# Kernel tuning notes

Measured on AMD Instinct MI355X. Metric: run time of the kernel, lower is better.

The kernel has to match this reference:

```python
import jax, jax.numpy as jnp
import numpy as np

DIM = 4096
HEADS = 32
HD = DIM // HEADS  # 128
SEQ = 2048
BSZ = 2
ALEN = 10
ROPE_THETA = 10000.0


def _make_freqs(seq, hd):
    inv = 1.0 / (ROPE_THETA ** (np.arange(0, hd, 2, dtype=np.float32) / hd))
    t = np.arange(seq, dtype=np.float32)
    ang = np.outer(t, inv)  # [seq, hd/2]
    return jnp.asarray(np.cos(ang)), jnp.asarray(np.sin(ang))


def setup_inputs() -> dict:
    key = jax.random.key(0)
    ks = jax.random.split(key, 8)
    s = 1.0 / np.sqrt(DIM)
    x = jax.random.normal(ks[0], (BSZ, SEQ, DIM), jnp.float32)
    wq = jax.random.normal(ks[1], (DIM, DIM), jnp.float32) * s  # [in, out]
    wk = jax.random.normal(ks[2], (DIM, DIM), jnp.float32) * s
    wv = jax.random.normal(ks[3], (DIM, DIM), jnp.float32) * s
    wo = jax.random.normal(ks[4], (DIM, DIM), jnp.float32) * s
    gate = 0.1 * jax.random.normal(ks[5], (1, HEADS, 1, 1), jnp.float32)
    adapter = jax.random.normal(ks[6], (1, ALEN, DIM), jnp.float32)
    freqs_cos, freqs_sin = _make_freqs(SEQ, HD)
    # causal additive mask, start_pos = 0
    mask = jnp.triu(jnp.full((1, 1, SEQ, SEQ), -1e9, jnp.float32), k=1)
    return {"x": x, "wq": wq, "wk": wk, "wv": wv, "wo": wo, "gate": gate,
            "adapter": adapter, "freqs_cos": freqs_cos, "freqs_sin": freqs_sin,
            "mask": mask, "start_pos": 0, "random_init": 0}


def _rope(t, cos, sin):
    # t: [b, s, H, hd]; cos/sin: [s, hd/2] -> broadcast (1, s, 1, hd/2)
    b, s, h, hd = t.shape
    t2 = t.reshape(b, s, h, hd // 2, 2)
    tr, ti = t2[..., 0], t2[..., 1]
    c = cos[None, :, None, :]
    sn = sin[None, :, None, :]
    orr = tr * c - ti * sn
    oi = tr * sn + ti * c
    return jnp.stack([orr, oi], axis=-1).reshape(b, s, h, hd)


def reference(x, wq, wk, wv, wo, gate, adapter, freqs_cos, freqs_sin, mask,
              start_pos, random_init):
    bsz, seqlen, dim = x.shape
    hd = 2 * freqs_cos.shape[-1]
    H = dim // hd
    L = adapter.shape[1]
    scale = 1.0 / jnp.sqrt(jnp.float32(hd))

    xq = (x @ wq).reshape(bsz, seqlen, H, hd)
    xk = (x @ wk).reshape(bsz, seqlen, H, hd)
    xv = (x @ wv).reshape(bsz, seqlen, H, hd)

    xq = _rope(xq, freqs_cos, freqs_sin)
    xk = _rope(xk, freqs_cos, freqs_sin)

    # adapter prefix K/V (no RoPE), shared across batch
    ak = (adapter @ wk).reshape(1, L, H, hd)  # [1, L, H, hd]
    av = (adapter @ wv).reshape(1, L, H, hd)

    # scores: normal keys masked causally; adapter keys unmasked (extra zeros)
    scores_n = jnp.einsum('bqhd,bkhd->bhqk', xq, xk) * scale + mask
    scores_a = jnp.einsum('bqhd,lhd->bhql', xq, ak[0]) * scale

    if random_init:
        # joint softmax over [adapter | normal] keys
        sc = jax.nn.softmax(jnp.concatenate([scores_a, scores_n], axis=-1), axis=-1)
        pa, pn = sc[..., :L], sc[..., L:]
    else:
        pa = jnp.tanh(gate) * jax.nn.softmax(scores_a, axis=-1)
        pn = jax.nn.softmax(scores_n, axis=-1)

    out = (jnp.einsum('bhql,lhd->bqhd', pa, av[0])
           + jnp.einsum('bhqk,bkhd->bqhd', pn, xv))
    out = out.reshape(bsz, seqlen, H * hd)
    return out @ wo
```

## Files before the change

kernel.cpp:

```cpp
#include <hip/hip_runtime.h>
#include <hip/hip_bf16.h>
#include <cstdint>

typedef float  f32x4  __attribute__((ext_vector_type(4)));
typedef __bf16 bf16x8 __attribute__((ext_vector_type(8)));
typedef __bf16 bf16x4 __attribute__((ext_vector_type(4)));
typedef __bf16 bf16x2 __attribute__((ext_vector_type(2)));

#define AS1 __attribute__((address_space(1)))
#define AS3 __attribute__((address_space(3)))

static constexpr int D   = 4096;
static constexpr int SEQ = 2048;
static constexpr int MX  = 4224;

__device__ __forceinline__ void gload_lds16(const void* g, void* l) {
  __builtin_amdgcn_global_load_lds((AS1 void*)(g), (AS3 void*)(l), 16, 0, 0);
}

__device__ __forceinline__ f32x4 mfma16(bf16x8 a, bf16x8 b, f32x4 c) {
  return __builtin_amdgcn_mfma_f32_16x16x32_bf16(a, b, c, 0, 0, 0);
}

__device__ __forceinline__ int xcd_chunk(int orig, int nwg) {
  int q = nwg >> 3, r = nwg & 7;
  int xcd = orig & 7, pos = orig >> 3;
  return (xcd < r ? xcd * (q + 1) : r * (q + 1) + (xcd - r) * q) + pos;
}

#define BARF() asm volatile("s_barrier" ::: "memory")

__global__ __launch_bounds__(256) void transpose_cast(const float* __restrict__ W,
                                                      __bf16* __restrict__ WT) {
  __shared__ float tile[64][65];
  const int t  = threadIdx.x;
  const int r0 = blockIdx.x * 64;
  const int c0 = blockIdx.y * 64;
#pragma unroll
  for (int p = 0; p < 4; ++p) {
    int e = p * 1024 + t * 4;
    int row = e >> 6, col = e & 63;
    f32x4 v = *(const f32x4*)(W + (size_t)(r0 + row) * D + c0 + col);
#pragma unroll
    for (int i = 0; i < 4; ++i) tile[row][col + i] = v[i];
  }
  __syncthreads();
#pragma unroll
  for (int p = 0; p < 2; ++p) {
    int e = p * 2048 + t * 8;
    int orow = e >> 6, ocol = e & 63;
    bf16x8 o;
#pragma unroll
    for (int i = 0; i < 8; ++i) o[i] = (__bf16)tile[ocol + i][orow];
    *(bf16x8*)(WT + (size_t)(c0 + orow) * D + r0 + ocol) = o;
  }
}

__global__ __launch_bounds__(256) void build_xa(const float* __restrict__ x,
                                                const float* __restrict__ ad,
                                                __bf16* __restrict__ xa) {
  int idx = blockIdx.x * 256 + threadIdx.x;
  int e = idx * 4;
  int row = e >> 12, col = e & 4095;
  f32x4 v = {};
  if (row < 4096)      v = *(const f32x4*)(x + (size_t)row * D + col);
  else if (row < 4106) v = *(const f32x4*)(ad + (size_t)(row - 4096) * D + col);
  bf16x4 o;
#pragma unroll
  for (int i = 0; i < 4; ++i) o[i] = (__bf16)v[i];
  *(bf16x4*)(xa + (size_t)row * D + col) = o;
}

template <int MODE>
__global__ __launch_bounds__(512, 2) void gemm256(const __bf16* __restrict__ A,
                                                  const __bf16* __restrict__ BT,
                                                  void* __restrict__ O0,
                                                  void* __restrict__ O1,
                                                  void* __restrict__ O2,
                                                  int Mt) {
  __shared__ __bf16 lds[65536];
  const int tid = threadIdx.x;
  const int wv = tid >> 6, ln = tid & 63;
  const int lg = ln >> 4, lr = ln & 15;

  const int nwg = gridDim.x;
  const int wgid = xcd_chunk(blockIdx.x, nwg);
  const int m0 = (wgid % Mt) * 256;
  const int n0 = (wgid / Mt) * 256;
  const int wm = (wv >> 2) * 128, wn = (wv & 3) * 64;

  auto stageHalf = [&](int k, int mat, int half) {
    const int slot = k & 1;
    const int kt = k * 64;
    const __bf16* base = mat ? BT + (size_t)(n0 + half * 128) * 4096
                             : A  + (size_t)(m0 + half * 128) * 4096;
#pragma unroll
    for (int i = 0; i < 2; ++i) {
      int c = i * 512 + tid;
      int r = c >> 3;
      int ch = (c & 7) ^ (r & 7);
      gload_lds16(base + (size_t)r * 4096 + kt + ch * 8,
                  lds + slot * 32768 + mat * 16384 + half * 8192 +
                      (i * 512 + wv * 64) * 8);
    }
  };

  f32x4 acc[8][4] = {};
  bf16x8 aLo[4][2], aHi[4][2], bLo[2][2], bHi[2][2];

  auto rdA = [&](const __bf16* pA, int mi, int kk) -> bf16x8 {
    int r = wm + mi * 16 + lr;
    int R = r & 127;
    int cw = (kk * 4 + lg) ^ (R & 7);
    return *(const bf16x8*)(pA + (r >> 7) * 8192 + R * 64 + cw * 8);
  };
  auto rdB = [&](const __bf16* pB, int ni, int kk) -> bf16x8 {
    int n = wn + ni * 16 + lr;
    int R = n & 127;
    int cw = (kk * 4 + lg) ^ (R & 7);
    return *(const bf16x8*)(pB + (n >> 7) * 8192 + R * 64 + cw * 8);
  };

  stageHalf(0, 0, 0);
  stageHalf(0, 1, 0);
  stageHalf(0, 0, 1);
  stageHalf(0, 1, 1);
  stageHalf(1, 0, 0);
  stageHalf(1, 1, 0);

  for (int k = 0; k < 63; ++k) {
    const int slot = k & 1;
    const __bf16* pA = lds + slot * 32768;
    const __bf16* pB = lds + slot * 32768 + 16384;

    stageHalf(k + 1, 0, 1);
    asm volatile("s_waitcnt vmcnt(8)" ::: "memory");
    BARF();
#pragma unroll
    for (int mi = 0; mi < 4; ++mi)
#pragma unroll
      for (int kk = 0; kk < 2; ++kk) aLo[mi][kk] = rdA(pA, mi, kk);
#pragma unroll
    for (int ni = 0; ni < 2; ++ni)
#pragma unroll
      for (int kk = 0; kk < 2; ++kk) bLo[ni][kk] = rdB(pB, ni, kk);
    __builtin_amdgcn_s_setprio(1);
#pragma unroll
    for (int kk = 0; kk < 2; ++kk)
#pragma unroll
      for (int mi = 0; mi < 4; ++mi)
#pragma unroll
        for (int ni = 0; ni < 2; ++ni)
          acc[mi][ni] = mfma16(aLo[mi][kk], bLo[ni][kk], acc[mi][ni]);
    __builtin_amdgcn_s_setprio(0);
    BARF();

    stageHalf(k + 1, 1, 1);
#pragma unroll
    for (int mi = 0; mi < 4; ++mi)
#pragma unroll
      for (int kk = 0; kk < 2; ++kk) aHi[mi][kk] = rdA(pA, mi + 4, kk);
    asm volatile("s_waitcnt vmcnt(8)" ::: "memory");
    BARF();
    __builtin_amdgcn_s_setprio(1);
#pragma unroll
    for (int kk = 0; kk < 2; ++kk)
#pragma unroll
      for (int mi = 0; mi < 4; ++mi)
#pragma unroll
        for (int ni = 0; ni < 2; ++ni)
          acc[mi + 4][ni] = mfma16(aHi[mi][kk], bLo[ni][kk], acc[mi + 4][ni]);
    __builtin_amdgcn_s_setprio(0);
    BARF();

    if (k + 2 < 64) stageHalf(k + 2, 0, 0);
#pragma unroll
    for (int ni = 0; ni < 2; ++ni)
#pragma unroll
      for (int kk = 0; kk < 2; ++kk) bHi[ni][kk] = rdB(pB, ni + 2, kk);
    BARF();
    __builtin_amdgcn_s_setprio(1);
#pragma unroll
    for (int kk = 0; kk < 2; ++kk)
#pragma unroll
      for (int mi = 0; mi < 4; ++mi)
#pragma unroll
        for (int ni = 0; ni < 2; ++ni)
          acc[mi + 4][ni + 2] = mfma16(aHi[mi][kk], bHi[ni][kk], acc[mi + 4][ni + 2]);
    __builtin_amdgcn_s_setprio(0);
    BARF();

    if (k + 2 < 64) stageHalf(k + 2, 1, 0);
    BARF();
    __builtin_amdgcn_s_setprio(1);
#pragma unroll
    for (int kk = 0; kk < 2; ++kk)
#pragma unroll
      for (int mi = 0; mi < 4; ++mi)
#pragma unroll
        for (int ni = 0; ni < 2; ++ni)
          acc[mi][ni + 2] = mfma16(aLo[mi][kk], bHi[ni][kk], acc[mi][ni + 2]);
    __builtin_amdgcn_s_setprio(0);
    BARF();
  }

  {
    const __bf16* pA = lds + (63 & 1) * 32768;
    const __bf16* pB = lds + (63 & 1) * 32768 + 16384;
    asm volatile("s_waitcnt vmcnt(0)" ::: "memory");
    BARF();
#pragma unroll
    for (int mi = 0; mi < 4; ++mi)
#pragma unroll
      for (int kk = 0; kk < 2; ++kk) aLo[mi][kk] = rdA(pA, mi, kk);
#pragma unroll
    for (int ni = 0; ni < 2; ++ni)
#pragma unroll
      for (int kk = 0; kk < 2; ++kk) bLo[ni][kk] = rdB(pB, ni, kk);
#pragma unroll
    for (int kk = 0; kk < 2; ++kk)
#pragma unroll
      for (int mi = 0; mi < 4; ++mi)
#pragma unroll
        for (int ni = 0; ni < 2; ++ni)
          acc[mi][ni] = mfma16(aLo[mi][kk], bLo[ni][kk], acc[mi][ni]);
#pragma unroll
    for (int mi = 0; mi < 4; ++mi)
#pragma unroll
      for (int kk = 0; kk < 2; ++kk) aHi[mi][kk] = rdA(pA, mi + 4, kk);
#pragma unroll
    for (int ni = 0; ni < 2; ++ni)
#pragma unroll
      for (int kk = 0; kk < 2; ++kk) bHi[ni][kk] = rdB(pB, ni + 2, kk);
#pragma unroll
    for (int kk = 0; kk < 2; ++kk)
#pragma unroll
      for (int mi = 0; mi < 4; ++mi)
#pragma unroll
        for (int ni = 0; ni < 2; ++ni) {
          acc[mi + 4][ni]     = mfma16(aHi[mi][kk], bLo[ni][kk], acc[mi + 4][ni]);
          acc[mi + 4][ni + 2] = mfma16(aHi[mi][kk], bHi[ni][kk], acc[mi + 4][ni + 2]);
          acc[mi][ni + 2]     = mfma16(aLo[mi][kk], bHi[ni][kk], acc[mi][ni + 2]);
        }
  }

  if constexpr (MODE == 0) {
    const int sel = n0 >> 12;
    __bf16* out = (sel == 0) ? (__bf16*)O0 : (sel == 1) ? (__bf16*)O1 : (__bf16*)O2;
    const int colb = n0 & 4095;
#pragma unroll
    for (int mi = 0; mi < 8; ++mi)
#pragma unroll
      for (int ni = 0; ni < 4; ++ni)
#pragma unroll
        for (int j = 0; j < 4; ++j) {
          int row = m0 + wm + mi * 16 + lg * 4 + j;
          int col = colb + wn + ni * 16 + lr;
          out[(size_t)row * 4096 + col] = (__bf16)acc[mi][ni][j];
        }
  } else {
    float* out = (float*)O0;
#pragma unroll
    for (int mi = 0; mi < 8; ++mi)
#pragma unroll
      for (int ni = 0; ni < 4; ++ni)
#pragma unroll
        for (int j = 0; j < 4; ++j) {
          int row = m0 + wm + mi * 16 + lg * 4 + j;
          int col = n0 + wn + ni * 16 + lr;
          out[(size_t)row * 4096 + col] = acc[mi][ni][j];
        }
  }
}

__global__ __launch_bounds__(256) void gemm_adapter(const __bf16* __restrict__ xa,
                                                    const __bf16* __restrict__ BT,
                                                    __bf16* __restrict__ kb,
                                                    __bf16* __restrict__ vb) {
  const int tid = threadIdx.x;
  const int wv = tid >> 6, ln = tid & 63;
  const int lg = ln >> 4, lr = ln & 15;
  const int col0 = blockIdx.x * 256 + wv * 64;
  f32x4 acc[4] = {};
  for (int kt = 0; kt < 4096; kt += 32) {
    bf16x8 a = *(const bf16x8*)(xa + (size_t)(4096 + lr) * 4096 + kt + lg * 8);
#pragma unroll
    for (int ni = 0; ni < 4; ++ni) {
      bf16x8 b = *(const bf16x8*)(BT + (size_t)(col0 + ni * 16 + lr) * 4096 +
                                  kt + lg * 8);
      acc[ni] = mfma16(a, b, acc[ni]);
    }
  }
#pragma unroll
  for (int ni = 0; ni < 4; ++ni)
#pragma unroll
    for (int j = 0; j < 4; ++j) {
      int row = 4096 + lg * 4 + j;
      int col = col0 + ni * 16 + lr;
      __bf16* out = (col < 4096) ? kb : vb;
      out[(size_t)row * 4096 + (col & 4095)] = (__bf16)acc[ni][j];
    }
}

__global__ __launch_bounds__(256) void rope_kernel(__bf16* __restrict__ q,
                                                   __bf16* __restrict__ k,
                                                   const float* __restrict__ fc,
                                                   const float* __restrict__ fs) {
  int row = blockIdx.x;
  __bf16* buf = blockIdx.y ? k : q;
  int t = threadIdx.x;
  int s = row & (SEQ - 1);
  int jb = (t & 7) * 8;
  const float* cp = fc + s * 64 + jb;
  const float* sp = fs + s * 64 + jb;
  __bf16* p = buf + (size_t)row * D + t * 16;
  bf16x8 v0 = *(const bf16x8*)p;
  bf16x8 v1 = *(const bf16x8*)(p + 8);
  bf16x8 o0, o1;
#pragma unroll
  for (int i = 0; i < 4; ++i) {
    float C = cp[i], Sn = sp[i];
    float re = (float)v0[2 * i], im = (float)v0[2 * i + 1];
    o0[2 * i]     = (__bf16)(re * C - im * Sn);
    o0[2 * i + 1] = (__bf16)(re * Sn + im * C);
  }
#pragma unroll
  for (int i = 0; i < 4; ++i) {
    float C = cp[4 + i], Sn = sp[4 + i];
    float re = (float)v1[2 * i], im = (float)v1[2 * i + 1];
    o1[2 * i]     = (__bf16)(re * C - im * Sn);
    o1[2 * i + 1] = (__bf16)(re * Sn + im * C);
  }
  *(bf16x8*)p = o0;
  *(bf16x8*)(p + 8) = o1;
}

__global__ __launch_bounds__(256) void transpose_v(const __bf16* __restrict__ V,
                                                   __bf16* __restrict__ VT) {
  __shared__ __bf16 tile[64][72];
  const int t  = threadIdx.x;
  const int r0 = blockIdx.x * 64;
  const int c0 = blockIdx.y * 64;
#pragma unroll
  for (int p = 0; p < 2; ++p) {
    int e = p * 2048 + t * 8;
    int row = e >> 6, col = e & 63;
    bf16x8 v8 = *(const bf16x8*)(V + (size_t)(r0 + row) * D + c0 + col);
#pragma unroll
    for (int i = 0; i < 8; ++i) tile[row][col + i] = v8[i];
  }
  __syncthreads();
#pragma unroll
  for (int p = 0; p < 2; ++p) {
    int e = p * 2048 + t * 8;
    int orow = e >> 6, ocol = e & 63;
    bf16x8 o;
#pragma unroll
    for (int i = 0; i < 8; ++i) o[i] = tile[ocol + i][orow];
    *(bf16x8*)(VT + (size_t)(c0 + orow) * MX + r0 + ocol) = o;
  }
}

__global__ __launch_bounds__(256) void attn_kernel(const __bf16* __restrict__ Q,
                                                   const __bf16* __restrict__ K,
                                                   const __bf16* __restrict__ VT,
                                                   const float* __restrict__ gate,
                                                   __bf16* __restrict__ Out) {
  __shared__ __bf16 Ks[2][64 * 128];
  __shared__ __bf16 Vs[2][128 * 64];
  __shared__ __bf16 Ps[4][32 * 64];

  const int tid = threadIdx.x;
  const int wv = tid >> 6, ln = tid & 63;
  const int lg = ln >> 4, lr = ln & 15;

  const int wgid = xcd_chunk(blockIdx.x, 512);
  const int px = wgid & 7;
  const int hb = wgid >> 3;
  const int h = hb & 31, b = hb >> 5;

  const float scale = 0.08838834764831845f;
  const float g = tanhf(gate[h]);

  auto stage = [&](int t, int buf) {
    const int kv0 = t * 64;
#pragma unroll
    for (int j = 0; j < 4; ++j) {
      int c = wv * 256 + j * 64 + ln;
      int rk = c >> 4, sck = (c & 15) ^ (rk & 7);
      gload_lds16(K + (size_t)(b * SEQ + kv0 + rk) * D + h * 128 + sck * 8,
                  Ks[buf] + (wv * 256 + j * 64) * 8);
      int rv = c >> 3, scv = (c & 7) ^ (rv & 7);
      gload_lds16(VT + (size_t)(h * 128 + rv) * MX + b * SEQ + kv0 + scv * 8,
                  Vs[buf] + (wv * 256 + j * 64) * 8);
    }
  };

  auto run_supertile = [&](int qt) {
    const int q0 = qt * 128;
    const int qbase = b * SEQ + q0 + wv * 32;

    bf16x8 qf[2][4];
#pragma unroll
    for (int mi = 0; mi < 2; ++mi)
#pragma unroll
      for (int kd = 0; kd < 4; ++kd)
        qf[mi][kd] = *(const bf16x8*)(Q + (size_t)(qbase + mi * 16 + lr) * D +
                                      h * 128 + kd * 32 + lg * 8);

    f32x4 O[2][8] = {};
    float mI2[2], lI2[2];
#pragma unroll
    for (int mi = 0; mi < 2; ++mi) { mI2[mi] = -1e30f; lI2[mi] = 0.f; }

    const int ntiles = 2 * qt + 2;
    stage(0, 0);

    for (int t = 0; t < ntiles; ++t) {
      const int cur = t & 1;
      const int kv0 = t * 64;
      if (t + 1 < ntiles) {
        stage(t + 1, cur ^ 1);
        asm volatile("s_waitcnt vmcnt(8)" ::: "memory");
      } else {
        asm volatile("s_waitcnt vmcnt(0)" ::: "memory");
      }
      __builtin_amdgcn_s_barrier();
      __builtin_amdgcn_sched_barrier(0);

      f32x4 S[2][4] = {};
      __builtin_amdgcn_s_setprio(1);
#pragma unroll
      for (int kd = 0; kd < 4; ++kd) {
        bf16x8 kf[4];
#pragma unroll
        for (int nf = 0; nf < 4; ++nf) {
          int kr = nf * 16 + lr;
          kf[nf] = *(const bf16x8*)(Ks[cur] + kr * 128 +
                                    (((kd * 4 + lg) ^ (kr & 7)) * 8));
        }
#pragma unroll
        for (int mi = 0; mi < 2; ++mi)
#pragma unroll
          for (int nf = 0; nf < 4; ++nf)
            S[mi][nf] = mfma16(kf[nf], qf[mi][kd], S[mi][nf]);
      }
      __builtin_amdgcn_s_setprio(0);

      float r2[2]; int grew = 0;
#pragma unroll
      for (int mi = 0; mi < 2; ++mi) {
        const int qg = q0 + wv * 32 + mi * 16 + lr;
        float mo = mI2[mi];
        float mt = -3e38f;
#pragma unroll
        for (int nf = 0; nf < 4; ++nf)
#pragma unroll
          for (int j = 0; j < 4; ++j) {
            int kvg = kv0 + nf * 16 + lg * 4 + j;
            float s = S[mi][nf][j] * scale;
            s = (kvg > qg) ? -1e30f : s;
            S[mi][nf][j] = s;
            mt = fmaxf(mt, s);
          }
        mt = fmaxf(mt, __shfl_xor(mt, 16));
        mt = fmaxf(mt, __shfl_xor(mt, 32));
        float mn = fmaxf(mo, mt);
        float ps = 0.f;
#pragma unroll
        for (int nf = 0; nf < 4; ++nf)
#pragma unroll
          for (int j = 0; j < 4; ++j) {
            float p = __expf(S[mi][nf][j] - mn);
            S[mi][nf][j] = p;
            ps += p;
          }
        ps += __shfl_xor(ps, 16);
        ps += __shfl_xor(ps, 32);
        float r = __expf(mo - mn);
        lI2[mi] = lI2[mi] * r + ps;
        mI2[mi] = mn;
        r2[mi] = r;
        grew |= (mn > mo) ? 1 : 0;
      }
      if (__any(grew)) {
#pragma unroll
        for (int mi = 0; mi < 2; ++mi)
#pragma unroll
          for (int j = 0; j < 4; ++j) {
            float rj = __shfl(r2[mi], lg * 4 + j);
#pragma unroll
            for (int n = 0; n < 8; ++n) O[mi][n][j] *= rj;
          }
      }

#pragma unroll
      for (int mi = 0; mi < 2; ++mi) {
        int q = mi * 16 + lr;
#pragma unroll
        for (int nf = 0; nf < 4; ++nf) {
          int kv = nf * 16 + lg * 4;
          bf16x4 pk;
#pragma unroll
          for (int j = 0; j < 4; ++j) pk[j] = (__bf16)S[mi][nf][j];
          *(bf16x4*)(Ps[wv] + q * 64 + (((kv >> 3) ^ (q & 7)) * 8) + (kv & 7)) = pk;
        }
      }

      __builtin_amdgcn_s_setprio(1);
#pragma unroll
      for (int kkv = 0; kkv < 2; ++kkv) {
        bf16x8 pf[2];
#pragma unroll
        for (int mi = 0; mi < 2; ++mi) {
          int prw = mi * 16 + lr;
          pf[mi] = *(const bf16x8*)(Ps[wv] + prw * 64 +
                                    (((kkv * 4 + lg) ^ (prw & 7)) * 8));
        }
#pragma unroll
        for (int n = 0; n < 8; ++n) {
          int vr = n * 16 + lr;
          bf16x8 vf = *(const bf16x8*)(Vs[cur] + vr * 64 +
                                       (((kkv * 4 + lg) ^ (vr & 7)) * 8));
#pragma unroll
          for (int mi = 0; mi < 2; ++mi) O[mi][n] = mfma16(pf[mi], vf, O[mi][n]);
        }
      }
      __builtin_amdgcn_s_setprio(0);

      __builtin_amdgcn_s_barrier();
      __builtin_amdgcn_sched_barrier(0);
    }

#pragma unroll
    for (int mi = 0; mi < 2; ++mi) {
      float inv = 1.0f / lI2[mi];
#pragma unroll
      for (int j = 0; j < 4; ++j) {
        float invj = __shfl(inv, lg * 4 + j);
#pragma unroll
        for (int n = 0; n < 8; ++n) O[mi][n][j] *= invj;
      }
    }

    {
      f32x4 Sa[2] = {};
#pragma unroll
      for (int kd = 0; kd < 4; ++kd) {
        bf16x8 kfa = *(const bf16x8*)(K + (size_t)(2 * SEQ + lr) * D +
                                      h * 128 + kd * 32 + lg * 8);
#pragma unroll
        for (int mi = 0; mi < 2; ++mi) Sa[mi] = mfma16(kfa, qf[mi][kd], Sa[mi]);
      }
#pragma unroll
      for (int mi = 0; mi < 2; ++mi) {
        float mt = -3e38f;
#pragma unroll
        for (int j = 0; j < 4; ++j) {
          int kv = lg * 4 + j;
          float s = Sa[mi][j] * scale;
          s = (kv >= 10) ? -1e30f : s;
          Sa[mi][j] = s;
          mt = fmaxf(mt, s);
        }
        mt = fmaxf(mt, __shfl_xor(mt, 16));
        mt = fmaxf(mt, __shfl_xor(mt, 32));
        float ps = 0.f;
#pragma unroll
        for (int j = 0; j < 4; ++j) {
          float p = __expf(Sa[mi][j] - mt);
          Sa[mi][j] = p;
          ps += p;
        }
        ps += __shfl_xor(ps, 16);
        ps += __shfl_xor(ps, 32);
        float gs = g / ps;
        int q = mi * 16 + lr;
        int kv = lg * 4;
        bf16x4 pk, z = {};
#pragma unroll
        for (int j = 0; j < 4; ++j) pk[j] = (__bf16)(Sa[mi][j] * gs);
        *(bf16x4*)(Ps[wv] + q * 64 + (((kv >> 3) ^ (q & 7)) * 8) + (kv & 7)) = pk;
        int kv2 = 16 + kv;
        *(bf16x4*)(Ps[wv] + q * 64 + (((kv2 >> 3) ^ (q & 7)) * 8) + (kv2 & 7)) = z;
      }
      bf16x8 pfa[2];
#pragma unroll
      for (int mi = 0; mi < 2; ++mi) {
        int prw = mi * 16 + lr;
        pfa[mi] = *(const bf16x8*)(Ps[wv] + prw * 64 + ((lg ^ (prw & 7)) * 8));
      }
#pragma unroll
      for (int n = 0; n < 8; ++n) {
        bf16x8 vfa = *(const bf16x8*)(VT + (size_t)(h * 128 + n * 16 + lr) * MX +
                                      2 * SEQ + lg * 8);
#pragma unroll
        for (int mi = 0; mi < 2; ++mi) O[mi][n] = mfma16(pfa[mi], vfa, O[mi][n]);
      }
    }

#pragma unroll
    for (int mi = 0; mi < 2; ++mi)
#pragma unroll
      for (int n = 0; n < 8; ++n)
#pragma unroll
        for (int j = 0; j < 4; ++j)
          Out[(size_t)(qbase + mi * 16 + lg * 4 + j) * D + h * 128 + n * 16 + lr] =
              (__bf16)O[mi][n][j];
  };

  run_supertile(15 - px);
  run_supertile(px);
}

extern "C" void kernel_launch(void* const* d_in, const int* in_sizes, int n_in,
                              void* d_out, int out_size, void* d_ws, size_t ws_size,
                              hipStream_t stream) {
  const float* x    = (const float*)d_in[0];
  const float* wq   = (const float*)d_in[1];
  const float* wk   = (const float*)d_in[2];
  const float* wv   = (const float*)d_in[3];
  const float* wo   = (const float*)d_in[4];
  const float* gate = (const float*)d_in[5];
  const float* ad   = (const float*)d_in[6];
  const float* fc   = (const float*)d_in[7];
  const float* fs   = (const float*)d_in[8];

  const size_t WSZ = (size_t)D * D * 2;
  const size_t XSZ = (size_t)MX * D * 2;
  if (ws_size < 4 * WSZ + XSZ + WSZ + 3 * XSZ) return;

  char* w = (char*)d_ws;
  size_t off = 0;
  auto alloc = [&](size_t sz) { void* p = w + off; off += sz; return p; };
  __bf16* wqT = (__bf16*)alloc(WSZ);
  __bf16* wkT = (__bf16*)alloc(WSZ);
  __bf16* wvT = (__bf16*)alloc(WSZ);
  __bf16* woT = (__bf16*)alloc(WSZ);
  __bf16* xa  = (__bf16*)alloc(XSZ);
  __bf16* qb  = (__bf16*)alloc(WSZ);
  __bf16* kb  = (__bf16*)alloc(XSZ);
  __bf16* vb  = (__bf16*)alloc(XSZ);
  __bf16* vT  = (__bf16*)alloc(XSZ);
  __bf16* attn = vb;

  dim3 blk(256);
  transpose_cast<<<dim3(64, 64), blk, 0, stream>>>(wq, wqT);
  transpose_cast<<<dim3(64, 64), blk, 0, stream>>>(wk, wkT);
  transpose_cast<<<dim3(64, 64), blk, 0, stream>>>(wv, wvT);
  transpose_cast<<<dim3(64, 64), blk, 0, stream>>>(wo, woT);
  build_xa<<<dim3(16896), blk, 0, stream>>>(x, ad, xa);

  gemm256<0><<<dim3(16 * 48), dim3(512), 0, stream>>>(xa, wqT, qb, kb, vb, 16);
  gemm_adapter<<<dim3(32), blk, 0, stream>>>(xa, wkT, kb, vb);

  rope_kernel<<<dim3(4096, 2), blk, 0, stream>>>(qb, kb, fc, fs);
  transpose_v<<<dim3(66, 64), blk, 0, stream>>>(vb, vT);

  attn_kernel<<<dim3(512), blk, 0, stream>>>(qb, kb, vT, gate, attn);

  gemm256<1><<<dim3(16 * 16), dim3(512), 0, stream>>>(attn, woT, d_out, nullptr, nullptr, 16);
}
```

Before: 850.8 us.

## Fuse RoPE and V transpose into QKV GEMM epilogue, batch weight transposes

Applies RoPE to Q and K inside the QKV GEMM epilogue, using a lane shuffle to pair real and imaginary parts. V is written straight into transposed layout, so the separate rope and transpose_v kernels and their round trips through global memory are removed. The four weight transpose-cast launches become one launch with a z dimension. In exchange the epilogue does more work, reads the frequency tables, and the transposed V stores are narrow strided writes that may coalesce poorly.

```diff
diff --git a/kernel.cpp b/kernel.cpp
--- a/kernel.cpp
+++ b/kernel.cpp
@@ -30,9 +30,15 @@
 
 #define BARF() asm volatile("s_barrier" ::: "memory")
 
-__global__ __launch_bounds__(256) void transpose_cast(const float* __restrict__ W,
-                                                      __bf16* __restrict__ WT) {
+__global__ __launch_bounds__(256) void transpose_cast4(const float* __restrict__ w0,
+                                                       const float* __restrict__ w1,
+                                                       const float* __restrict__ w2,
+                                                       const float* __restrict__ w3,
+                                                       __bf16* __restrict__ WT) {
   __shared__ float tile[64][65];
+  const float* W = (blockIdx.z == 0) ? w0 : (blockIdx.z == 1) ? w1
+                 : (blockIdx.z == 2) ? w2 : w3;
+  __bf16* dst = WT + (size_t)blockIdx.z * D * D;
   const int t  = threadIdx.x;
   const int r0 = blockIdx.x * 64;
   const int c0 = blockIdx.y * 64;
@@ -52,7 +58,7 @@
     bf16x8 o;
 #pragma unroll
     for (int i = 0; i < 8; ++i) o[i] = (__bf16)tile[ocol + i][orow];
-    *(bf16x8*)(WT + (size_t)(c0 + orow) * D + r0 + ocol) = o;
+    *(bf16x8*)(dst + (size_t)(c0 + orow) * D + r0 + ocol) = o;
   }
 }
 
@@ -77,6 +83,8 @@
                                                   void* __restrict__ O0,
                                                   void* __restrict__ O1,
                                                   void* __restrict__ O2,
+                                                  const float* __restrict__ FC,
+                                                  const float* __restrict__ FS,
                                                   int Mt) {
   __shared__ __bf16 lds[65536];
   const int tid = threadIdx.x;
@@ -246,18 +254,42 @@
 
   if constexpr (MODE == 0) {
     const int sel = n0 >> 12;
-    __bf16* out = (sel == 0) ? (__bf16*)O0 : (sel == 1) ? (__bf16*)O1 : (__bf16*)O2;
     const int colb = n0 & 4095;
-#pragma unroll
-    for (int mi = 0; mi < 8; ++mi)
-#pragma unroll
-      for (int ni = 0; ni < 4; ++ni)
+    if (sel < 2) {
+      __bf16* out = sel ? (__bf16*)O1 : (__bf16*)O0;
+#pragma unroll
+      for (int mi = 0; mi < 8; ++mi)
 #pragma unroll
         for (int j = 0; j < 4; ++j) {
           int row = m0 + wm + mi * 16 + lg * 4 + j;
+          int s = row & (SEQ - 1);
+#pragma unroll
+          for (int ni = 0; ni < 4; ++ni) {
+            int col = colb + wn + ni * 16 + lr;
+            int fi = (col & 127) >> 1;
+            float c  = FC[s * 64 + fi];
+            float sn = FS[s * 64 + fi];
+            float v = acc[mi][ni][j];
+            float p = __shfl_xor(v, 1);
+            float o = (lr & 1) ? (p * sn + v * c) : (v * c - p * sn);
+            out[(size_t)row * 4096 + col] = (__bf16)o;
+          }
+        }
+    } else {
+      __bf16* vT = (__bf16*)O2;
+#pragma unroll
+      for (int mi = 0; mi < 8; ++mi) {
+        int row0 = m0 + wm + mi * 16 + lg * 4;
+#pragma unroll
+        for (int ni = 0; ni < 4; ++ni) {
           int col = colb + wn + ni * 16 + lr;
-          out[(size_t)row * 4096 + col] = (__bf16)acc[mi][ni][j];
-        }
+          bf16x4 pk;
+#pragma unroll
+          for (int j = 0; j < 4; ++j) pk[j] = (__bf16)acc[mi][ni][j];
+          *(bf16x4*)(vT + (size_t)col * MX + row0) = pk;
+        }
+      }
+    }
   } else {
     float* out = (float*)O0;
 #pragma unroll
@@ -276,7 +308,7 @@
 __global__ __launch_bounds__(256) void gemm_adapter(const __bf16* __restrict__ xa,
                                                     const __bf16* __restrict__ BT,
                                                     __bf16* __restrict__ kb,
-                                                    __bf16* __restrict__ vb) {
+                                                    __bf16* __restrict__ vT) {
   const int tid = threadIdx.x;
   const int wv = tid >> 6, ln = tid & 63;
   const int lg = ln >> 4, lr = ln & 15;
@@ -297,68 +329,9 @@
     for (int j = 0; j < 4; ++j) {
       int row = 4096 + lg * 4 + j;
       int col = col0 + ni * 16 + lr;
-      __bf16* out = (col < 4096) ? kb : vb;
-      out[(size_t)row * 4096 + (col & 4095)] = (__bf16)acc[ni][j];
-    }
-}
-
-__global__ __launch_bounds__(256) void rope_kernel(__bf16* __restrict__ q,
-                                                   __bf16* __restrict__ k,
-                                                   const float* __restrict__ fc,
-                                                   const float* __restrict__ fs) {
-  int row = blockIdx.x;
-  __bf16* buf = blockIdx.y ? k : q;
-  int t = threadIdx.x;
-  int s = row & (SEQ - 1);
-  int jb = (t & 7) * 8;
-  const float* cp = fc + s * 64 + jb;
-  const float* sp = fs + s * 64 + jb;
-  __bf16* p = buf + (size_t)row * D + t * 16;
-  bf16x8 v0 = *(const bf16x8*)p;
-  bf16x8 v1 = *(const bf16x8*)(p + 8);
-  bf16x8 o0, o1;
-#pragma unroll
-  for (int i = 0; i < 4; ++i) {
-    float C = cp[i], Sn = sp[i];
-    float re = (float)v0[2 * i], im = (float)v0[2 * i + 1];
-    o0[2 * i]     = (__bf16)(re * C - im * Sn);
-    o0[2 * i + 1] = (__bf16)(re * Sn + im * C);
-  }
-#pragma unroll
-  for (int i = 0; i < 4; ++i) {
-    float C = cp[4 + i], Sn = sp[4 + i];
-    float re = (float)v1[2 * i], im = (float)v1[2 * i + 1];
-    o1[2 * i]     = (__bf16)(re * C - im * Sn);
-    o1[2 * i + 1] = (__bf16)(re * Sn + im * C);
-  }
-  *(bf16x8*)p = o0;
-  *(bf16x8*)(p + 8) = o1;
-}
-
-__global__ __launch_bounds__(256) void transpose_v(const __bf16* __restrict__ V,
-                                                   __bf16* __restrict__ VT) {
-  __shared__ __bf16 tile[64][72];
-  const int t  = threadIdx.x;
-  const int r0 = blockIdx.x * 64;
-  const int c0 = blockIdx.y * 64;
-#pragma unroll
-  for (int p = 0; p < 2; ++p) {
-    int e = p * 2048 + t * 8;
-    int row = e >> 6, col = e & 63;
-    bf16x8 v8 = *(const bf16x8*)(V + (size_t)(r0 + row) * D + c0 + col);
-#pragma unroll
-    for (int i = 0; i < 8; ++i) tile[row][col + i] = v8[i];
-  }
-  __syncthreads();
-#pragma unroll
-  for (int p = 0; p < 2; ++p) {
-    int e = p * 2048 + t * 8;
-    int orow = e >> 6, ocol = e & 63;
-    bf16x8 o;
-#pragma unroll
-    for (int i = 0; i < 8; ++i) o[i] = tile[ocol + i][orow];
-    *(bf16x8*)(VT + (size_t)(c0 + orow) * MX + r0 + ocol) = o;
-  }
+      if (col < 4096) kb[(size_t)row * 4096 + col] = (__bf16)acc[ni][j];
+      else            vT[(size_t)(col & 4095) * MX + row] = (__bf16)acc[ni][j];
+    }
 }
 
 __global__ __launch_bounds__(256) void attn_kernel(const __bf16* __restrict__ Q,
@@ -643,21 +616,19 @@
   __bf16* vb  = (__bf16*)alloc(XSZ);
   __bf16* vT  = (__bf16*)alloc(XSZ);
   __bf16* attn = vb;
+  (void)wkT; (void)wvT;
 
   dim3 blk(256);
-  transpose_cast<<<dim3(64, 64), blk, 0, stream>>>(wq, wqT);
-  transpose_cast<<<dim3(64, 64), blk, 0, stream>>>(wk, wkT);
-  transpose_cast<<<dim3(64, 64), blk, 0, stream>>>(wv, wvT);
-  transpose_cast<<<dim3(64, 64), blk, 0, stream>>>(wo, woT);
+  transpose_cast4<<<dim3(64, 64, 4), blk, 0, stream>>>(wq, wk, wv, wo, wqT);
   build_xa<<<dim3(16896), blk, 0, stream>>>(x, ad, xa);
 
-  gemm256<0><<<dim3(16 * 48), dim3(512), 0, stream>>>(xa, wqT, qb, kb, vb, 16);
-  gemm_adapter<<<dim3(32), blk, 0, stream>>>(xa, wkT, kb, vb);
-
-  rope_kernel<<<dim3(4096, 2), blk, 0, stream>>>(qb, kb, fc, fs);
-  transpose_v<<<dim3(66, 64), blk, 0, stream>>>(vb, vT);
+  gemm256<0><<<dim3(16 * 48), dim3(512), 0, stream>>>(xa, wqT, qb, kb, vT,
+                                                      fc, fs, 16);
+  gemm_adapter<<<dim3(32), blk, 0, stream>>>(xa, wkT, kb, vT);
 
   attn_kernel<<<dim3(512), blk, 0, stream>>>(qb, kb, vT, gate, attn);
 
-  gemm256<1><<<dim3(16 * 16), dim3(512), 0, stream>>>(attn, woT, d_out, nullptr, nullptr, 16);
-}
+  gemm256<1><<<dim3(16 * 16), dim3(512), 0, stream>>>(attn, woT, d_out,
+                                                      nullptr, nullptr,
+                                                      nullptr, nullptr, 16);
+}
```

Measured after the change: 824.1 us. 3.1% less time.
